# Performance work log

Measured on AMD Instinct MI355X. Metric: run time of the kernel, lower is better.

The kernel has to match this reference:

```python
import jax, jax.numpy as jnp
import numpy as np

N_NODES = 100000
N_EDGES = 3200000
N_GRAPHS = 512


def setup_inputs() -> dict:
    key = jax.random.key(0)
    k1, k2, k3, k4, k5 = jax.random.split(key, 5)
    x = jax.random.normal(k1, (N_NODES, 5), dtype=jnp.float32)
    edge_index = jax.random.randint(k2, (2, N_EDGES), 0, N_NODES, dtype=jnp.int64)
    batch = jnp.sort(jax.random.randint(k3, (N_NODES,), 0, N_GRAPHS, dtype=jnp.int64))
    W1 = jax.random.normal(k4, (5, 16), dtype=jnp.float32) * (1.0 / np.sqrt(5.0))
    b1 = jnp.zeros((16,), dtype=jnp.float32)
    W2 = jax.random.normal(k5, (16, 16), dtype=jnp.float32) * 0.25
    b2 = jnp.zeros((16,), dtype=jnp.float32)
    return {"x": x, "edge_index": edge_index, "batch": batch,
            "W1": W1, "b1": b1, "W2": W2, "b2": b2}


def _gcn_conv(x, src, dst, norm, W, b, n_nodes):
    # PyG GCNConv: h = X W; out_i = sum_{j->i} norm_ij * h_j + b
    h = x @ W                                   # [N, out]
    msgs = h[src] * norm[:, None]               # gather + scale  [E_tot, out]
    out = jax.ops.segment_sum(msgs, dst, num_segments=n_nodes)
    return out + b


def reference(x, edge_index, batch, W1, b1, W2, b2):
    n = x.shape[0]
    # add self-loops (GCNConv default)
    loops = jnp.arange(n, dtype=edge_index.dtype)
    src = jnp.concatenate([edge_index[0], loops])
    dst = jnp.concatenate([edge_index[1], loops])
    # symmetric normalization: deg computed on destination nodes
    deg = jax.ops.segment_sum(jnp.ones_like(src, dtype=x.dtype), dst, num_segments=n)
    dinv = jnp.where(deg > 0, jax.lax.rsqrt(deg), 0.0)
    norm = dinv[src] * dinv[dst]                # [E_tot]

    h = jax.nn.relu(_gcn_conv(x, src, dst, norm, W1, b1, n))
    h = jax.nn.relu(_gcn_conv(h, src, dst, norm, W2, b2, n))

    # global mean pool over graphs in the batch
    sums = jax.ops.segment_sum(h, batch, num_segments=N_GRAPHS)
    cnts = jax.ops.segment_sum(jnp.ones((n,), dtype=h.dtype), batch, num_segments=N_GRAPHS)
    return sums / jnp.maximum(cnts, 1.0)[:, None]
```

## Files before the change

### kernel.cpp

```cpp
#include <hip/hip_runtime.h>

#define N_NODES  100000
#define N_EDGES  3200000
#define N_GRAPHS 512
#define F_IN     5
#define F_HID    16

#define PBLK   512
#define CHUNK  4096
#define EPT    (CHUNK / PBLK)
#define NCHUNK ((N_EDGES + CHUNK - 1) / CHUNK)
#define CNT_NODES 128
#define BKT_NODES 256
#define NBKT ((N_NODES + BKT_NODES - 1) / BKT_NODES)
#define SHARDS 8
#define CAP_S  1280
#define CAP    (SHARDS * CAP_S)
#define UNR    (CAP / 512)


__device__ inline unsigned short f2bf(float f) {
    unsigned u = __float_as_uint(f);
    return (unsigned short)((u + 0x7fffu + ((u >> 16) & 1u)) >> 16);
}
__device__ inline float bf2f(unsigned short h) {
    return __uint_as_float(((unsigned)h) << 16);
}
__device__ inline float4 cvt4(ushort4 u) {
    return make_float4(bf2f(u.x), bf2f(u.y), bf2f(u.z), bf2f(u.w));
}
__device__ inline float4 shfl_xor4(float4 v, int m) {
    return make_float4(__shfl_xor(v.x, m, 64), __shfl_xor(v.y, m, 64),
                       __shfl_xor(v.z, m, 64), __shfl_xor(v.w, m, 64));
}

template <int NW>
__device__ inline int block_incl_scan(int v, int t, int* wsum) {
    int lane = t & 63, wave = t >> 6;
    int x = v;
#pragma unroll
    for (int o = 1; o < 64; o <<= 1) {
        int y = __shfl_up(x, o, 64);
        if (lane >= o) x += y;
    }
    if (lane == 63) wsum[wave] = x;
    __syncthreads();
    if (t < 64) {
        int w = (t < NW) ? wsum[t] : 0;
#pragma unroll
        for (int o = 1; o < NW; o <<= 1) {
            int y = __shfl_up(w, o, 64);
            if (t >= o) w += y;
        }
        if (t < NW) wsum[t] = w;
    }
    __syncthreads();
    return x + (wave ? wsum[wave - 1] : 0);
}

__device__ inline float4 row_gather8s(const ushort4* __restrict__ pb4, int i, int j,
                                      int half, int beg, int len,
                                      const int* __restrict__ col) {
    float4 acc = half ? make_float4(0.f, 0.f, 0.f, 0.f)
                      : cvt4(pb4[i * 4 + j]);
    for (int k = half * 8; k < len; k += 16) {
        int4 c0 = *(const int4*)(col + beg + k);
        int4 c1 = *(const int4*)(col + beg + k + 4);
        ushort4 a0 = pb4[c0.x * 4 + j], a1 = pb4[c0.y * 4 + j];
        ushort4 a2 = pb4[c0.z * 4 + j], a3 = pb4[c0.w * 4 + j];
        ushort4 a4 = pb4[c1.x * 4 + j], a5 = pb4[c1.y * 4 + j];
        ushort4 a6 = pb4[c1.z * 4 + j], a7 = pb4[c1.w * 4 + j];
        float4 f0 = cvt4(a0), f1 = cvt4(a1), f2 = cvt4(a2), f3 = cvt4(a3);
        float4 f4 = cvt4(a4), f5 = cvt4(a5), f6 = cvt4(a6), f7 = cvt4(a7);
        acc.x += ((f0.x + f1.x) + (f2.x + f3.x)) + ((f4.x + f5.x) + (f6.x + f7.x));
        acc.y += ((f0.y + f1.y) + (f2.y + f3.y)) + ((f4.y + f5.y) + (f6.y + f7.y));
        acc.z += ((f0.z + f1.z) + (f2.z + f3.z)) + ((f4.z + f5.z) + (f6.z + f7.z));
        acc.w += ((f0.w + f1.w) + (f2.w + f3.w)) + ((f4.w + f5.w) + (f6.w + f7.w));
    }
    return acc;
}


__global__ void k_zero(int* __restrict__ cursor, float* __restrict__ out,
                       float* __restrict__ cnt, unsigned short* __restrict__ pb_a,
                       unsigned short* __restrict__ pb_b) {
    int i = blockIdx.x * blockDim.x + threadIdx.x;
    if (i < NBKT * SHARDS) cursor[i] = 0;
    if (i < N_GRAPHS * F_HID) out[i] = 0.0f;
    if (i < N_GRAPHS) cnt[i] = 0.0f;
    if (i < F_HID) {
        pb_a[(size_t)N_NODES * F_HID + i] = 0;
        pb_b[(size_t)N_NODES * F_HID + i] = 0;
    }
}

__global__ __launch_bounds__(PBLK) void k_part(const int* __restrict__ src,
                                               const int* __restrict__ dst,
                                               const int* __restrict__ batch,
                                               int* __restrict__ cursor,
                                               unsigned* __restrict__ packed,
                                               float* __restrict__ cnt) {
    __shared__ int hist[PBLK];
    __shared__ int gbase[PBLK];
    __shared__ int bcnt[8];
    __shared__ int g0s;
    int t = threadIdx.x;
    int blk = blockIdx.x;
    int s = blk & (SHARDS - 1);
    int chunk0 = blk * CHUNK;
    int n = min(CHUNK, N_EDGES - chunk0);
    hist[t] = 0;
    if (t < 8) bcnt[t] = 0;
    if (t == 0) {
        int nb = blk * CNT_NODES;
        g0s = batch[nb < N_NODES ? nb : N_NODES - 1];
    }
    __syncthreads();
    int ls[EPT], ld[EPT], lr[EPT];
#pragma unroll
    for (int idx = 0; idx < EPT; idx++) {
        int k = t + idx * PBLK;
        if (k < n) {
            ls[idx] = src[chunk0 + k];
            ld[idx] = dst[chunk0 + k];
            lr[idx] = atomicAdd(&hist[ld[idx] >> 8], 1);
        }
    }
    if (t < CNT_NODES) {
        int i2 = blk * CNT_NODES + t;
        if (i2 < N_NODES) {
            int g = batch[i2];
            int l = g - g0s;
            if (l >= 0 && l < 8) atomicAdd(&bcnt[l], 1);
            else atomicAdd(&cnt[g], 1.0f);
        }
    }
    __syncthreads();
    int v = hist[t];
    gbase[t] = (v > 0) ? atomicAdd(&cursor[t * SHARDS + s], v) : 0;
    if (t < 8 && bcnt[t] > 0) atomicAdd(&cnt[g0s + t], (float)bcnt[t]);
    __syncthreads();
#pragma unroll
    for (int idx = 0; idx < EPT; idx++) {
        int k = t + idx * PBLK;
        if (k < n) {
            int b = ld[idx] >> 8;
            int g = gbase[b] + lr[idx];
            if (g < CAP_S)
                packed[(size_t)b * CAP + s * CAP_S + g] =
                    ((unsigned)ls[idx] << 8) | (unsigned)(ld[idx] & 255);
        }
    }
}

__global__ __launch_bounds__(512) void k_csr(const int* __restrict__ cursor,
                                             const unsigned* __restrict__ packed,
                                             const float* __restrict__ x,
                                             const float* __restrict__ W1,
                                             int2* __restrict__ rowbc,
                                             int* __restrict__ col,
                                             float* __restrict__ dinv,
                                             unsigned short* __restrict__ pb) {
    __shared__ int hist[BKT_NODES];
    __shared__ int excl_s[BKT_NODES];
    __shared__ int wsum[8];
    __shared__ int ns[SHARDS];
    __shared__ float w1[F_IN * F_HID];
    int b = blockIdx.x, t = threadIdx.x;
    int base = b * CAP;
    if (t < BKT_NODES) hist[t] = 0;
    if (t < SHARDS) ns[t] = min(cursor[b * SHARDS + t], CAP_S);
    if (t < F_IN * F_HID) w1[t] = W1[t];
    __syncthreads();
    const unsigned* pk = packed + (size_t)b * CAP;
    unsigned pv[UNR];
    int pr[UNR];
    unsigned okm = 0;
#pragma unroll
    for (int idx = 0; idx < UNR; idx++) {
        int k = t + idx * 512;
        int sh = k / CAP_S;
        if ((k - sh * CAP_S) < ns[sh]) {
            okm |= (1u << idx);
            pv[idx] = pk[k];
            pr[idx] = atomicAdd(&hist[pv[idx] & 255], 1);
        }
    }
    __syncthreads();
    int v = (t < BKT_NODES) ? hist[t] : 0;
    int len = (v + 7) & ~7;
    int incl = block_incl_scan<8>(len, t, wsum);
    int excl = incl - len;
    if (t < BKT_NODES) excl_s[t] = excl;
    __syncthreads();
#pragma unroll
    for (int idx = 0; idx < UNR; idx++) {
        if (okm & (1u << idx)) {
            unsigned w = pv[idx];
            int r = excl_s[w & 255] + pr[idx];
            if (r < CAP) col[base + r] = (int)(w >> 8);
        }
    }
    if (t < BKT_NODES) {
        int node = b * BKT_NODES + t;
        if (node < N_NODES) {
            int mylen = min(len, ((CAP - min(excl, CAP)) & ~7));
            for (int q = v; q < mylen; q++) {
                int r = excl + q;
                if (r < CAP) col[base + r] = N_NODES;
            }
            rowbc[node] = make_int2(base + excl, mylen);
            float di = rsqrtf((float)(1 + v));
            dinv[node] = di;
            float xi[F_IN];
#pragma unroll
            for (int k = 0; k < F_IN; k++) xi[k] = x[node * F_IN + k];
            float hv[F_HID];
#pragma unroll
            for (int c = 0; c < F_HID; c++) {
                float h = 0.0f;
#pragma unroll
                for (int k = 0; k < F_IN; k++) h += xi[k] * w1[k * F_HID + c];
                hv[c] = h * di;
            }
            unsigned pkk[8];
#pragma unroll
            for (int q = 0; q < 8; q++)
                pkk[q] = (unsigned)f2bf(hv[2 * q]) | ((unsigned)f2bf(hv[2 * q + 1]) << 16);
            uint4* d4 = (uint4*)(pb + (size_t)node * F_HID);
            d4[0] = make_uint4(pkk[0], pkk[1], pkk[2], pkk[3]);
            d4[1] = make_uint4(pkk[4], pkk[5], pkk[6], pkk[7]);
        }
    }
}

__global__ __launch_bounds__(256) void k_pull_mid(const int2* __restrict__ rowbc,
                                                  const int* __restrict__ col,
                                                  const unsigned short* __restrict__ pb,
                                                  const float* __restrict__ dinv,
                                                  const float* __restrict__ W2,
                                                  const float* __restrict__ b1,
                                                  unsigned short* __restrict__ pb2) {
    __shared__ float w[F_HID * F_HID];
    __shared__ float bb[F_HID];
    int t = threadIdx.x;
    w[t] = W2[t];
    if (t < F_HID) bb[t] = b1[t];
    __syncthreads();
    int gid = blockIdx.x * 256 + t;
    int i = gid >> 3;
    int half = (gid >> 2) & 1;
    int j = gid & 3;
    int2 rc = rowbc[i];
    float4 acc = row_gather8s((const ushort4*)pb, i, j, half, rc.x, rc.y, col);
    acc.x += __shfl_xor(acc.x, 4, 64);
    acc.y += __shfl_xor(acc.y, 4, 64);
    acc.z += __shfl_xor(acc.z, 4, 64);
    acc.w += __shfl_xor(acc.w, 4, 64);
    float di = dinv[i];
    float4 mine;
    mine.x = fmaxf(di * acc.x + bb[4 * j + 0], 0.0f);
    mine.y = fmaxf(di * acc.y + bb[4 * j + 1], 0.0f);
    mine.z = fmaxf(di * acc.z + bb[4 * j + 2], 0.0f);
    mine.w = fmaxf(di * acc.w + bb[4 * j + 3], 0.0f);
    float4 o1 = shfl_xor4(mine, 1);
    float4 o2 = shfl_xor4(mine, 2);
    float4 o3 = shfl_xor4(mine, 3);
    float4 hq0 = (j == 0) ? mine : ((j == 1) ? o1 : ((j == 2) ? o2 : o3));
    float4 hq1 = (j == 1) ? mine : ((j == 0) ? o1 : ((j == 3) ? o2 : o3));
    float4 hq2 = (j == 2) ? mine : ((j == 3) ? o1 : ((j == 0) ? o2 : o3));
    float4 hq3 = (j == 3) ? mine : ((j == 2) ? o1 : ((j == 1) ? o2 : o3));
    float hc[F_HID] = {hq0.x, hq0.y, hq0.z, hq0.w, hq1.x, hq1.y, hq1.z, hq1.w,
                       hq2.x, hq2.y, hq2.z, hq2.w, hq3.x, hq3.y, hq3.z, hq3.w};
    float m0 = 0.0f, m1 = 0.0f, m2 = 0.0f, m3 = 0.0f;
#pragma unroll
    for (int c = 0; c < F_HID; c++) {
        float4 wv = *(const float4*)&w[c * F_HID + 4 * j];
        float hv = hc[c];
        m0 += hv * wv.x; m1 += hv * wv.y; m2 += hv * wv.z; m3 += hv * wv.w;
    }
    if (half == 0) {
        unsigned p0 = (unsigned)f2bf(m0 * di) | ((unsigned)f2bf(m1 * di) << 16);
        unsigned p1 = (unsigned)f2bf(m2 * di) | ((unsigned)f2bf(m3 * di) << 16);
        *(uint2*)(pb2 + (size_t)i * F_HID + 4 * j) = make_uint2(p0, p1);
    }
}

__global__ __launch_bounds__(256) void k_pull_pool(const int2* __restrict__ rowbc,
                                                   const int* __restrict__ col,
                                                   const unsigned short* __restrict__ pb,
                                                   const float* __restrict__ dinv,
                                                   const int* __restrict__ batch,
                                                   const float* __restrict__ b2,
                                                   const float* __restrict__ cnt,
                                                   float* __restrict__ out) {
    __shared__ float bb[F_HID];
    __shared__ float acc2[8][F_HID];
    __shared__ int gcnt[8];
    __shared__ int g0s;
    int t = threadIdx.x;
    if (t < F_HID) bb[t] = b2[t];
    if (t < 8) gcnt[t] = 0;
    if (t < 8 * F_HID) ((float*)acc2)[t] = 0.0f;
    int blk0node = blockIdx.x * 32;
    if (t == 0) g0s = batch[blk0node < N_NODES ? blk0node : N_NODES - 1];
    __syncthreads();
    int g0 = g0s;
    int gid = blockIdx.x * 256 + t;
    int i = gid >> 3;
    int half = (gid >> 2) & 1;
    int j = gid & 3;
    int2 rc = rowbc[i];
    float4 acc = row_gather8s((const ushort4*)pb, i, j, half, rc.x, rc.y, col);
    acc.x += __shfl_xor(acc.x, 4, 64);
    acc.y += __shfl_xor(acc.y, 4, 64);
    acc.z += __shfl_xor(acc.z, 4, 64);
    acc.w += __shfl_xor(acc.w, 4, 64);
    if (half == 0) {
        float di = dinv[i];
        float h0 = fmaxf(di * acc.x + bb[4 * j + 0], 0.0f);
        float h1 = fmaxf(di * acc.y + bb[4 * j + 1], 0.0f);
        float h2 = fmaxf(di * acc.z + bb[4 * j + 2], 0.0f);
        float h3 = fmaxf(di * acc.w + bb[4 * j + 3], 0.0f);
        int g = batch[i];
        int l = g - g0;
        if (l >= 0 && l < 8) {
            atomicAdd(&acc2[l][4 * j + 0], h0);
            atomicAdd(&acc2[l][4 * j + 1], h1);
            atomicAdd(&acc2[l][4 * j + 2], h2);
            atomicAdd(&acc2[l][4 * j + 3], h3);
            if (j == 0) atomicAdd(&gcnt[l], 1);
        } else {
            float inv = 1.0f / cnt[g];
            atomicAdd(&out[g * F_HID + 4 * j + 0], h0 * inv);
            atomicAdd(&out[g * F_HID + 4 * j + 1], h1 * inv);
            atomicAdd(&out[g * F_HID + 4 * j + 2], h2 * inv);
            atomicAdd(&out[g * F_HID + 4 * j + 3], h3 * inv);
        }
    }
    __syncthreads();
    if (t < 8 * F_HID) {
        int l = t >> 4, c = t & 15;
        if (gcnt[l] > 0) {
            float inv = 1.0f / cnt[g0 + l];
            atomicAdd(&out[(g0 + l) * F_HID + c], acc2[l][c] * inv);
        }
    }
}


extern "C" void kernel_launch(void* const* d_in, const int* in_sizes, int n_in,
                              void* d_out, int out_size, void* d_ws, size_t ws_size,
                              hipStream_t stream) {
    const float* x     = (const float*)d_in[0];
    const int*   ei    = (const int*)d_in[1];
    const int*   batch = (const int*)d_in[2];
    const float* W1    = (const float*)d_in[3];
    const float* b1    = (const float*)d_in[4];
    const float* W2    = (const float*)d_in[5];
    const float* b2    = (const float*)d_in[6];
    float* out = (float*)d_out;

    int*            cursor = (int*)d_ws;
    unsigned*       packed = (unsigned*)(cursor + 3200);
    int2*           rowbc  = (int2*)(packed + (size_t)NBKT * CAP);
    int*            col    = (int*)(rowbc + N_NODES);
    float*          dinv   = (float*)(col + (size_t)NBKT * CAP);
    unsigned short* pb_a   = (unsigned short*)(dinv + N_NODES);
    unsigned short* pb_b   = pb_a + (size_t)(N_NODES + 1) * F_HID;
    float*          cnt    = (float*)(pb_b + (size_t)(N_NODES + 1) * F_HID);

    const int* src = ei;
    const int* dst = ei + N_EDGES;

    const int nb_pull = (N_NODES * 8) / 256;

    k_zero<<<(N_GRAPHS * F_HID + 255) / 256, 256, 0, stream>>>(cursor, out, cnt,
                                                               pb_a, pb_b);
    k_part<<<NCHUNK, PBLK, 0, stream>>>(src, dst, batch, cursor, packed, cnt);
    k_csr<<<NBKT, 512, 0, stream>>>(cursor, packed, x, W1, rowbc, col, dinv, pb_a);
    k_pull_mid<<<nb_pull, 256, 0, stream>>>(rowbc, col, pb_a, dinv, W2, b1, pb_b);
    k_pull_pool<<<nb_pull, 256, 0, stream>>>(rowbc, col, pb_b, dinv, batch, b2,
                                             cnt, out);
}
```

Before: 190.0 us.

## Fuse GCN pipeline into one cooperative persistent kernel with grid syncs

Merges the zero, partition, CSR-build and two pull kernels into a single cooperative kernel. The phases are separated by grid.sync, and persistent blocks loop over chunks, buckets and windows. The goal is to remove the launch and inter-kernel drain gaps between the five stages. Buckets and chunks are halved, blocks drop to 256 threads, and CSR construction now reads packed edges twice with atomic ranking instead of caching them in registers. Risks include grid-sync cost, lower occupancy from capping resident blocks at four per CU during the latency-bound gather phases, and the extra packed reads; a non-cooperative multi-kernel fallback is kept.

```diff
diff --git a/kernel.cpp b/kernel.cpp
--- a/kernel.cpp
+++ b/kernel.cpp
@@ -1,4 +1,7 @@
 #include <hip/hip_runtime.h>
+#include <hip/hip_cooperative_groups.h>
+
+namespace cg = cooperative_groups;
 
 #define N_NODES  100000
 #define N_EDGES  3200000
@@ -6,17 +9,18 @@
 #define F_IN     5
 #define F_HID    16
 
-#define PBLK   512
-#define CHUNK  4096
-#define EPT    (CHUNK / PBLK)
+#define NTHR   256
+#define CHUNK  2048
+#define EPT    (CHUNK / NTHR)
 #define NCHUNK ((N_EDGES + CHUNK - 1) / CHUNK)
-#define CNT_NODES 128
-#define BKT_NODES 256
+#define CNT_NODES 64
+#define BKT_NODES 128
+#define BKT_SHIFT 7
 #define NBKT ((N_NODES + BKT_NODES - 1) / BKT_NODES)
 #define SHARDS 8
-#define CAP_S  1280
+#define CAP_S  768
 #define CAP    (SHARDS * CAP_S)
-#define UNR    (CAP / 512)
+#define NWIN   (N_NODES / 32)
 
 
 __device__ inline unsigned short f2bf(float f) {
@@ -34,8 +38,7 @@
                        __shfl_xor(v.z, m, 64), __shfl_xor(v.w, m, 64));
 }
 
-template <int NW>
-__device__ inline int block_incl_scan(int v, int t, int* wsum) {
+__device__ inline int scan128(int v, int t, int* wsum) {
     int lane = t & 63, wave = t >> 6;
     int x = v;
 #pragma unroll
@@ -46,13 +49,13 @@
     if (lane == 63) wsum[wave] = x;
     __syncthreads();
     if (t < 64) {
-        int w = (t < NW) ? wsum[t] : 0;
-#pragma unroll
-        for (int o = 1; o < NW; o <<= 1) {
+        int w = (t < 4) ? wsum[t] : 0;
+#pragma unroll
+        for (int o = 1; o < 4; o <<= 1) {
             int y = __shfl_up(w, o, 64);
             if (t >= o) w += y;
         }
-        if (t < NW) wsum[t] = w;
+        if (t < 4) wsum[t] = w;
     }
     __syncthreads();
     return x + (wave ? wsum[wave - 1] : 0);
@@ -81,53 +84,39 @@
 }
 
 
-__global__ void k_zero(int* __restrict__ cursor, float* __restrict__ out,
-                       float* __restrict__ cnt, unsigned short* __restrict__ pb_a,
-                       unsigned short* __restrict__ pb_b) {
-    int i = blockIdx.x * blockDim.x + threadIdx.x;
-    if (i < NBKT * SHARDS) cursor[i] = 0;
-    if (i < N_GRAPHS * F_HID) out[i] = 0.0f;
-    if (i < N_GRAPHS) cnt[i] = 0.0f;
-    if (i < F_HID) {
-        pb_a[(size_t)N_NODES * F_HID + i] = 0;
-        pb_b[(size_t)N_NODES * F_HID + i] = 0;
-    }
-}
-
-__global__ __launch_bounds__(PBLK) void k_part(const int* __restrict__ src,
-                                               const int* __restrict__ dst,
-                                               const int* __restrict__ batch,
-                                               int* __restrict__ cursor,
-                                               unsigned* __restrict__ packed,
-                                               float* __restrict__ cnt) {
-    __shared__ int hist[PBLK];
-    __shared__ int gbase[PBLK];
+__device__ inline void phase_part(int c, const int* __restrict__ src,
+                                  const int* __restrict__ dst,
+                                  const int* __restrict__ batch,
+                                  int* __restrict__ cursor,
+                                  unsigned* __restrict__ packed,
+                                  float* __restrict__ cnt) {
+    __shared__ int hist[NBKT];
+    __shared__ int gbase[NBKT];
     __shared__ int bcnt[8];
     __shared__ int g0s;
     int t = threadIdx.x;
-    int blk = blockIdx.x;
-    int s = blk & (SHARDS - 1);
-    int chunk0 = blk * CHUNK;
+    int s = c & (SHARDS - 1);
+    int chunk0 = c * CHUNK;
     int n = min(CHUNK, N_EDGES - chunk0);
-    hist[t] = 0;
+    for (int i = t; i < NBKT; i += NTHR) hist[i] = 0;
     if (t < 8) bcnt[t] = 0;
     if (t == 0) {
-        int nb = blk * CNT_NODES;
+        int nb = c * CNT_NODES;
         g0s = batch[nb < N_NODES ? nb : N_NODES - 1];
     }
     __syncthreads();
     int ls[EPT], ld[EPT], lr[EPT];
 #pragma unroll
     for (int idx = 0; idx < EPT; idx++) {
-        int k = t + idx * PBLK;
+        int k = t + idx * NTHR;
         if (k < n) {
             ls[idx] = src[chunk0 + k];
             ld[idx] = dst[chunk0 + k];
-            lr[idx] = atomicAdd(&hist[ld[idx] >> 8], 1);
+            lr[idx] = atomicAdd(&hist[ld[idx] >> BKT_SHIFT], 1);
         }
     }
     if (t < CNT_NODES) {
-        int i2 = blk * CNT_NODES + t;
+        int i2 = c * CNT_NODES + t;
         if (i2 < N_NODES) {
             int g = batch[i2];
             int l = g - g0s;
@@ -136,69 +125,68 @@
         }
     }
     __syncthreads();
-    int v = hist[t];
-    gbase[t] = (v > 0) ? atomicAdd(&cursor[t * SHARDS + s], v) : 0;
+    for (int b = t; b < NBKT; b += NTHR) {
+        int v = hist[b];
+        gbase[b] = (v > 0) ? atomicAdd(&cursor[b * SHARDS + s], v) : 0;
+    }
     if (t < 8 && bcnt[t] > 0) atomicAdd(&cnt[g0s + t], (float)bcnt[t]);
     __syncthreads();
 #pragma unroll
     for (int idx = 0; idx < EPT; idx++) {
-        int k = t + idx * PBLK;
+        int k = t + idx * NTHR;
         if (k < n) {
-            int b = ld[idx] >> 8;
+            int b = ld[idx] >> BKT_SHIFT;
             int g = gbase[b] + lr[idx];
             if (g < CAP_S)
                 packed[(size_t)b * CAP + s * CAP_S + g] =
-                    ((unsigned)ls[idx] << 8) | (unsigned)(ld[idx] & 255);
-        }
-    }
-}
-
-__global__ __launch_bounds__(512) void k_csr(const int* __restrict__ cursor,
-                                             const unsigned* __restrict__ packed,
-                                             const float* __restrict__ x,
-                                             const float* __restrict__ W1,
-                                             int2* __restrict__ rowbc,
-                                             int* __restrict__ col,
-                                             float* __restrict__ dinv,
-                                             unsigned short* __restrict__ pb) {
-    __shared__ int hist[BKT_NODES];
-    __shared__ int excl_s[BKT_NODES];
-    __shared__ int wsum[8];
+                    ((unsigned)ls[idx] << BKT_SHIFT) |
+                    (unsigned)(ld[idx] & (BKT_NODES - 1));
+        }
+    }
+    __syncthreads();
+}
+
+__device__ inline void phase_csr(int b, const int* __restrict__ cursor,
+                                 const unsigned* __restrict__ packed,
+                                 const float* __restrict__ x,
+                                 const float* __restrict__ W1,
+                                 int2* __restrict__ rowbc, int* __restrict__ col,
+                                 float* __restrict__ dinv,
+                                 unsigned short* __restrict__ pb) {
+    __shared__ int chist[BKT_NODES];
+    __shared__ int crnk[BKT_NODES];
+    __shared__ int wsum[4];
     __shared__ int ns[SHARDS];
     __shared__ float w1[F_IN * F_HID];
-    int b = blockIdx.x, t = threadIdx.x;
+    int t = threadIdx.x;
     int base = b * CAP;
-    if (t < BKT_NODES) hist[t] = 0;
+    if (t < BKT_NODES) chist[t] = 0;
     if (t < SHARDS) ns[t] = min(cursor[b * SHARDS + t], CAP_S);
     if (t < F_IN * F_HID) w1[t] = W1[t];
     __syncthreads();
     const unsigned* pk = packed + (size_t)b * CAP;
-    unsigned pv[UNR];
-    int pr[UNR];
-    unsigned okm = 0;
-#pragma unroll
-    for (int idx = 0; idx < UNR; idx++) {
-        int k = t + idx * 512;
-        int sh = k / CAP_S;
-        if ((k - sh * CAP_S) < ns[sh]) {
-            okm |= (1u << idx);
-            pv[idx] = pk[k];
-            pr[idx] = atomicAdd(&hist[pv[idx] & 255], 1);
-        }
-    }
-    __syncthreads();
-    int v = (t < BKT_NODES) ? hist[t] : 0;
+#pragma unroll
+    for (int s = 0; s < SHARDS; s++) {
+        int m = ns[s];
+        const unsigned* pks = pk + s * CAP_S;
+        for (int k = t; k < m; k += NTHR)
+            atomicAdd(&chist[pks[k] & (BKT_NODES - 1)], 1);
+    }
+    __syncthreads();
+    int v = (t < BKT_NODES) ? chist[t] : 0;
     int len = (v + 7) & ~7;
-    int incl = block_incl_scan<8>(len, t, wsum);
+    int incl = scan128(len, t, wsum);
     int excl = incl - len;
-    if (t < BKT_NODES) excl_s[t] = excl;
-    __syncthreads();
-#pragma unroll
-    for (int idx = 0; idx < UNR; idx++) {
-        if (okm & (1u << idx)) {
-            unsigned w = pv[idx];
-            int r = excl_s[w & 255] + pr[idx];
-            if (r < CAP) col[base + r] = (int)(w >> 8);
+    if (t < BKT_NODES) crnk[t] = excl;
+    __syncthreads();
+#pragma unroll
+    for (int s = 0; s < SHARDS; s++) {
+        int m = ns[s];
+        const unsigned* pks = pk + s * CAP_S;
+        for (int k = t; k < m; k += NTHR) {
+            unsigned w = pks[k];
+            int r = atomicAdd(&crnk[w & (BKT_NODES - 1)], 1);
+            if (r < CAP) col[base + r] = (int)(w >> BKT_SHIFT);
         }
     }
     if (t < BKT_NODES) {
@@ -226,31 +214,31 @@
             unsigned pkk[8];
 #pragma unroll
             for (int q = 0; q < 8; q++)
-                pkk[q] = (unsigned)f2bf(hv[2 * q]) | ((unsigned)f2bf(hv[2 * q + 1]) << 16);
+                pkk[q] = (unsigned)f2bf(hv[2 * q]) |
+                         ((unsigned)f2bf(hv[2 * q + 1]) << 16);
             uint4* d4 = (uint4*)(pb + (size_t)node * F_HID);
             d4[0] = make_uint4(pkk[0], pkk[1], pkk[2], pkk[3]);
             d4[1] = make_uint4(pkk[4], pkk[5], pkk[6], pkk[7]);
         }
     }
-}
-
-__global__ __launch_bounds__(256) void k_pull_mid(const int2* __restrict__ rowbc,
-                                                  const int* __restrict__ col,
-                                                  const unsigned short* __restrict__ pb,
-                                                  const float* __restrict__ dinv,
-                                                  const float* __restrict__ W2,
-                                                  const float* __restrict__ b1,
-                                                  unsigned short* __restrict__ pb2) {
-    __shared__ float w[F_HID * F_HID];
-    __shared__ float bb[F_HID];
+    __syncthreads();
+}
+
+__device__ inline void phase_mid(int w, const int2* __restrict__ rowbc,
+                                 const int* __restrict__ col,
+                                 const unsigned short* __restrict__ pb,
+                                 const float* __restrict__ dinv,
+                                 const float* __restrict__ W2,
+                                 const float* __restrict__ b1,
+                                 unsigned short* __restrict__ pb2) {
+    __shared__ float w2s[F_HID * F_HID];
+    __shared__ float bb1[F_HID];
     int t = threadIdx.x;
-    w[t] = W2[t];
-    if (t < F_HID) bb[t] = b1[t];
-    __syncthreads();
-    int gid = blockIdx.x * 256 + t;
-    int i = gid >> 3;
-    int half = (gid >> 2) & 1;
-    int j = gid & 3;
+    w2s[t] = W2[t];
+    if (t < F_HID) bb1[t] = b1[t];
+    __syncthreads();
+    int half = (t >> 2) & 1, j = t & 3, nl = t >> 3;
+    int i = w * 32 + nl;
     int2 rc = rowbc[i];
     float4 acc = row_gather8s((const ushort4*)pb, i, j, half, rc.x, rc.y, col);
     acc.x += __shfl_xor(acc.x, 4, 64);
@@ -259,10 +247,10 @@
     acc.w += __shfl_xor(acc.w, 4, 64);
     float di = dinv[i];
     float4 mine;
-    mine.x = fmaxf(di * acc.x + bb[4 * j + 0], 0.0f);
-    mine.y = fmaxf(di * acc.y + bb[4 * j + 1], 0.0f);
-    mine.z = fmaxf(di * acc.z + bb[4 * j + 2], 0.0f);
-    mine.w = fmaxf(di * acc.w + bb[4 * j + 3], 0.0f);
+    mine.x = fmaxf(di * acc.x + bb1[4 * j + 0], 0.0f);
+    mine.y = fmaxf(di * acc.y + bb1[4 * j + 1], 0.0f);
+    mine.z = fmaxf(di * acc.z + bb1[4 * j + 2], 0.0f);
+    mine.w = fmaxf(di * acc.w + bb1[4 * j + 3], 0.0f);
     float4 o1 = shfl_xor4(mine, 1);
     float4 o2 = shfl_xor4(mine, 2);
     float4 o3 = shfl_xor4(mine, 3);
@@ -275,7 +263,7 @@
     float m0 = 0.0f, m1 = 0.0f, m2 = 0.0f, m3 = 0.0f;
 #pragma unroll
     for (int c = 0; c < F_HID; c++) {
-        float4 wv = *(const float4*)&w[c * F_HID + 4 * j];
+        float4 wv = *(const float4*)&w2s[c * F_HID + 4 * j];
         float hv = hc[c];
         m0 += hv * wv.x; m1 += hv * wv.y; m2 += hv * wv.z; m3 += hv * wv.w;
     }
@@ -284,32 +272,30 @@
         unsigned p1 = (unsigned)f2bf(m2 * di) | ((unsigned)f2bf(m3 * di) << 16);
         *(uint2*)(pb2 + (size_t)i * F_HID + 4 * j) = make_uint2(p0, p1);
     }
-}
-
-__global__ __launch_bounds__(256) void k_pull_pool(const int2* __restrict__ rowbc,
-                                                   const int* __restrict__ col,
-                                                   const unsigned short* __restrict__ pb,
-                                                   const float* __restrict__ dinv,
-                                                   const int* __restrict__ batch,
-                                                   const float* __restrict__ b2,
-                                                   const float* __restrict__ cnt,
-                                                   float* __restrict__ out) {
-    __shared__ float bb[F_HID];
+    __syncthreads();
+}
+
+__device__ inline void phase_pool(int w, const int2* __restrict__ rowbc,
+                                  const int* __restrict__ col,
+                                  const unsigned short* __restrict__ pb,
+                                  const float* __restrict__ dinv,
+                                  const int* __restrict__ batch,
+                                  const float* __restrict__ b2,
+                                  const float* __restrict__ cnt,
+                                  float* __restrict__ out) {
+    __shared__ float bb2[F_HID];
     __shared__ float acc2[8][F_HID];
     __shared__ int gcnt[8];
-    __shared__ int g0s;
+    __shared__ int pg0;
     int t = threadIdx.x;
-    if (t < F_HID) bb[t] = b2[t];
+    if (t < F_HID) bb2[t] = b2[t];
     if (t < 8) gcnt[t] = 0;
     if (t < 8 * F_HID) ((float*)acc2)[t] = 0.0f;
-    int blk0node = blockIdx.x * 32;
-    if (t == 0) g0s = batch[blk0node < N_NODES ? blk0node : N_NODES - 1];
-    __syncthreads();
-    int g0 = g0s;
-    int gid = blockIdx.x * 256 + t;
-    int i = gid >> 3;
-    int half = (gid >> 2) & 1;
-    int j = gid & 3;
+    if (t == 0) pg0 = batch[w * 32];
+    __syncthreads();
+    int g0 = pg0;
+    int half = (t >> 2) & 1, j = t & 3, nl = t >> 3;
+    int i = w * 32 + nl;
     int2 rc = rowbc[i];
     float4 acc = row_gather8s((const ushort4*)pb, i, j, half, rc.x, rc.y, col);
     acc.x += __shfl_xor(acc.x, 4, 64);
@@ -318,10 +304,10 @@
     acc.w += __shfl_xor(acc.w, 4, 64);
     if (half == 0) {
         float di = dinv[i];
-        float h0 = fmaxf(di * acc.x + bb[4 * j + 0], 0.0f);
-        float h1 = fmaxf(di * acc.y + bb[4 * j + 1], 0.0f);
-        float h2 = fmaxf(di * acc.z + bb[4 * j + 2], 0.0f);
-        float h3 = fmaxf(di * acc.w + bb[4 * j + 3], 0.0f);
+        float h0 = fmaxf(di * acc.x + bb2[4 * j + 0], 0.0f);
+        float h1 = fmaxf(di * acc.y + bb2[4 * j + 1], 0.0f);
+        float h2 = fmaxf(di * acc.z + bb2[4 * j + 2], 0.0f);
+        float h3 = fmaxf(di * acc.w + bb2[4 * j + 3], 0.0f);
         int g = batch[i];
         int l = g - g0;
         if (l >= 0 && l < 8) {
@@ -346,6 +332,77 @@
             atomicAdd(&out[(g0 + l) * F_HID + c], acc2[l][c] * inv);
         }
     }
+    __syncthreads();
+}
+
+
+__global__ __launch_bounds__(NTHR, 4)
+void k_fused(const int* src, const int* dst, const int* batch, const float* x,
+             const float* W1, const float* b1, const float* W2, const float* b2,
+             int* cursor, unsigned* packed, int2* rowbc, int* col, float* dinv,
+             unsigned short* pb_a, unsigned short* pb_b, float* cnt, float* out) {
+    cg::grid_group grid = cg::this_grid();
+    int bid = blockIdx.x, t = threadIdx.x, nblk = gridDim.x;
+    int gstep = nblk * NTHR, gidx = bid * NTHR + t;
+    for (int i = gidx; i < NBKT * SHARDS; i += gstep) cursor[i] = 0;
+    for (int i = gidx; i < N_GRAPHS * F_HID; i += gstep) out[i] = 0.0f;
+    for (int i = gidx; i < N_GRAPHS; i += gstep) cnt[i] = 0.0f;
+    for (int i = gidx; i < F_HID; i += gstep) {
+        pb_a[(size_t)N_NODES * F_HID + i] = 0;
+        pb_b[(size_t)N_NODES * F_HID + i] = 0;
+    }
+    grid.sync();
+    for (int c = bid; c < NCHUNK; c += nblk)
+        phase_part(c, src, dst, batch, cursor, packed, cnt);
+    grid.sync();
+    for (int b = bid; b < NBKT; b += nblk)
+        phase_csr(b, cursor, packed, x, W1, rowbc, col, dinv, pb_a);
+    grid.sync();
+    for (int w = bid; w < NWIN; w += nblk)
+        phase_mid(w, rowbc, col, pb_a, dinv, W2, b1, pb_b);
+    grid.sync();
+    for (int w = bid; w < NWIN; w += nblk)
+        phase_pool(w, rowbc, col, pb_b, dinv, batch, b2, cnt, out);
+}
+
+
+__global__ __launch_bounds__(NTHR) void k_zero_s(int* cursor, float* out, float* cnt,
+                                                 unsigned short* pb_a,
+                                                 unsigned short* pb_b) {
+    int i = blockIdx.x * NTHR + threadIdx.x;
+    if (i < NBKT * SHARDS) cursor[i] = 0;
+    if (i < N_GRAPHS * F_HID) out[i] = 0.0f;
+    if (i < N_GRAPHS) cnt[i] = 0.0f;
+    if (i < F_HID) {
+        pb_a[(size_t)N_NODES * F_HID + i] = 0;
+        pb_b[(size_t)N_NODES * F_HID + i] = 0;
+    }
+}
+__global__ __launch_bounds__(NTHR) void k_part_s(const int* src, const int* dst,
+                                                 const int* batch, int* cursor,
+                                                 unsigned* packed, float* cnt) {
+    phase_part(blockIdx.x, src, dst, batch, cursor, packed, cnt);
+}
+__global__ __launch_bounds__(NTHR) void k_csr_s(const int* cursor,
+                                                const unsigned* packed,
+                                                const float* x, const float* W1,
+                                                int2* rowbc, int* col, float* dinv,
+                                                unsigned short* pb) {
+    phase_csr(blockIdx.x, cursor, packed, x, W1, rowbc, col, dinv, pb);
+}
+__global__ __launch_bounds__(NTHR) void k_mid_s(const int2* rowbc, const int* col,
+                                                const unsigned short* pb,
+                                                const float* dinv, const float* W2,
+                                                const float* b1,
+                                                unsigned short* pb2) {
+    phase_mid(blockIdx.x, rowbc, col, pb, dinv, W2, b1, pb2);
+}
+__global__ __launch_bounds__(NTHR) void k_pool_s(const int2* rowbc, const int* col,
+                                                 const unsigned short* pb,
+                                                 const float* dinv, const int* batch,
+                                                 const float* b2, const float* cnt,
+                                                 float* out) {
+    phase_pool(blockIdx.x, rowbc, col, pb, dinv, batch, b2, cnt, out);
 }
 
 
@@ -362,7 +419,7 @@
     float* out = (float*)d_out;
 
     int*            cursor = (int*)d_ws;
-    unsigned*       packed = (unsigned*)(cursor + 3200);
+    unsigned*       packed = (unsigned*)(cursor + 6400);
     int2*           rowbc  = (int2*)(packed + (size_t)NBKT * CAP);
     int*            col    = (int*)(rowbc + N_NODES);
     float*          dinv   = (float*)(col + (size_t)NBKT * CAP);
@@ -373,13 +430,29 @@
     const int* src = ei;
     const int* dst = ei + N_EDGES;
 
-    const int nb_pull = (N_NODES * 8) / 256;
-
-    k_zero<<<(N_GRAPHS * F_HID + 255) / 256, 256, 0, stream>>>(cursor, out, cnt,
-                                                               pb_a, pb_b);
-    k_part<<<NCHUNK, PBLK, 0, stream>>>(src, dst, batch, cursor, packed, cnt);
-    k_csr<<<NBKT, 512, 0, stream>>>(cursor, packed, x, W1, rowbc, col, dinv, pb_a);
-    k_pull_mid<<<nb_pull, 256, 0, stream>>>(rowbc, col, pb_a, dinv, W2, b1, pb_b);
-    k_pull_pool<<<nb_pull, 256, 0, stream>>>(rowbc, col, pb_b, dinv, batch, b2,
-                                             cnt, out);
-}
+    bool ok = false;
+    int maxBlk = 0;
+    hipError_t qe = hipOccupancyMaxActiveBlocksPerMultiprocessor(&maxBlk, k_fused,
+                                                                 NTHR, 0);
+    if (qe == hipSuccess && maxBlk > 0) {
+        int nblk = maxBlk * 256;
+        if (nblk > 1024) nblk = 1024;
+        void* args[] = {(void*)&src, (void*)&dst, (void*)&batch, (void*)&x,
+                        (void*)&W1, (void*)&b1, (void*)&W2, (void*)&b2,
+                        (void*)&cursor, (void*)&packed, (void*)&rowbc, (void*)&col,
+                        (void*)&dinv, (void*)&pb_a, (void*)&pb_b, (void*)&cnt,
+                        (void*)&out};
+        ok = hipLaunchCooperativeKernel((void*)k_fused, dim3(nblk), dim3(NTHR),
+                                        args, 0, stream) == hipSuccess;
+    }
+    if (!ok) {
+        k_zero_s<<<(N_GRAPHS * F_HID + NTHR - 1) / NTHR, NTHR, 0, stream>>>(
+            cursor, out, cnt, pb_a, pb_b);
+        k_part_s<<<NCHUNK, NTHR, 0, stream>>>(src, dst, batch, cursor, packed, cnt);
+        k_csr_s<<<NBKT, NTHR, 0, stream>>>(cursor, packed, x, W1, rowbc, col,
+                                           dinv, pb_a);
+        k_mid_s<<<NWIN, NTHR, 0, stream>>>(rowbc, col, pb_a, dinv, W2, b1, pb_b);
+        k_pool_s<<<NWIN, NTHR, 0, stream>>>(rowbc, col, pb_b, dinv, batch, b2,
+                                            cnt, out);
+    }
+}
```

Measured after the change: 524.4 us. 2.76x slower.

## Replicate bf16 feature tables per XCD and make CSR build two-pass

Applied to the files above, without the earlier changes.

Each bf16 node-feature table is now written as eight identical copies. Each gather block reads the copy chosen by blockIdx & 7, which lines up with the round-robin block-to-XCD assignment, so each XCD's L2 sees only its own copy. The goal is less cross-XCD contention on shared lines during the random row gathers, paid for with eight times the feature write traffic and workspace. Separately, k_csr stops holding packed edges in registers and rereads them in a second pass that places each edge with shared-memory atomics, and k_part's histogram is shrunk to the real bucket count.

```diff
diff --git a/kernel.cpp b/kernel.cpp
--- a/kernel.cpp
+++ b/kernel.cpp
@@ -17,6 +17,8 @@
 #define CAP_S  1280
 #define CAP    (SHARDS * CAP_S)
 #define UNR    (CAP / 512)
+#define NCOPY  8
+#define PBSTRIDE ((size_t)(N_NODES + 1) * F_HID)
 
 
 __device__ inline unsigned short f2bf(float f) {
@@ -88,9 +90,10 @@
     if (i < NBKT * SHARDS) cursor[i] = 0;
     if (i < N_GRAPHS * F_HID) out[i] = 0.0f;
     if (i < N_GRAPHS) cnt[i] = 0.0f;
-    if (i < F_HID) {
-        pb_a[(size_t)N_NODES * F_HID + i] = 0;
-        pb_b[(size_t)N_NODES * F_HID + i] = 0;
+    if (i < F_HID * NCOPY) {
+        int c = i / F_HID, q = i % F_HID;
+        pb_a[c * PBSTRIDE + (size_t)N_NODES * F_HID + q] = 0;
+        pb_b[c * PBSTRIDE + (size_t)N_NODES * F_HID + q] = 0;
     }
 }
 
@@ -100,8 +103,8 @@
                                                int* __restrict__ cursor,
                                                unsigned* __restrict__ packed,
                                                float* __restrict__ cnt) {
-    __shared__ int hist[PBLK];
-    __shared__ int gbase[PBLK];
+    __shared__ int hist[NBKT];
+    __shared__ int gbase[NBKT];
     __shared__ int bcnt[8];
     __shared__ int g0s;
     int t = threadIdx.x;
@@ -109,7 +112,7 @@
     int s = blk & (SHARDS - 1);
     int chunk0 = blk * CHUNK;
     int n = min(CHUNK, N_EDGES - chunk0);
-    hist[t] = 0;
+    if (t < NBKT) hist[t] = 0;
     if (t < 8) bcnt[t] = 0;
     if (t == 0) {
         int nb = blk * CNT_NODES;
@@ -136,8 +139,10 @@
         }
     }
     __syncthreads();
-    int v = hist[t];
-    gbase[t] = (v > 0) ? atomicAdd(&cursor[t * SHARDS + s], v) : 0;
+    if (t < NBKT) {
+        int v = hist[t];
+        gbase[t] = (v > 0) ? atomicAdd(&cursor[t * SHARDS + s], v) : 0;
+    }
     if (t < 8 && bcnt[t] > 0) atomicAdd(&cnt[g0s + t], (float)bcnt[t]);
     __syncthreads();
 #pragma unroll
@@ -162,7 +167,7 @@
                                              float* __restrict__ dinv,
                                              unsigned short* __restrict__ pb) {
     __shared__ int hist[BKT_NODES];
-    __shared__ int excl_s[BKT_NODES];
+    __shared__ int rnk[BKT_NODES];
     __shared__ int wsum[8];
     __shared__ int ns[SHARDS];
     __shared__ float w1[F_IN * F_HID];
@@ -173,31 +178,27 @@
     if (t < F_IN * F_HID) w1[t] = W1[t];
     __syncthreads();
     const unsigned* pk = packed + (size_t)b * CAP;
-    unsigned pv[UNR];
-    int pr[UNR];
-    unsigned okm = 0;
-#pragma unroll
-    for (int idx = 0; idx < UNR; idx++) {
-        int k = t + idx * 512;
-        int sh = k / CAP_S;
-        if ((k - sh * CAP_S) < ns[sh]) {
-            okm |= (1u << idx);
-            pv[idx] = pk[k];
-            pr[idx] = atomicAdd(&hist[pv[idx] & 255], 1);
-        }
+#pragma unroll
+    for (int s = 0; s < SHARDS; s++) {
+        int m = ns[s];
+        const unsigned* pks = pk + s * CAP_S;
+        for (int k = t; k < m; k += 512)
+            atomicAdd(&hist[pks[k] & 255], 1);
     }
     __syncthreads();
     int v = (t < BKT_NODES) ? hist[t] : 0;
     int len = (v + 7) & ~7;
     int incl = block_incl_scan<8>(len, t, wsum);
     int excl = incl - len;
-    if (t < BKT_NODES) excl_s[t] = excl;
-    __syncthreads();
-#pragma unroll
-    for (int idx = 0; idx < UNR; idx++) {
-        if (okm & (1u << idx)) {
-            unsigned w = pv[idx];
-            int r = excl_s[w & 255] + pr[idx];
+    if (t < BKT_NODES) rnk[t] = excl;
+    __syncthreads();
+#pragma unroll
+    for (int s = 0; s < SHARDS; s++) {
+        int m = ns[s];
+        const unsigned* pks = pk + s * CAP_S;
+        for (int k = t; k < m; k += 512) {
+            unsigned w = pks[k];
+            int r = atomicAdd(&rnk[w & 255], 1);
             if (r < CAP) col[base + r] = (int)(w >> 8);
         }
     }
@@ -227,9 +228,14 @@
 #pragma unroll
             for (int q = 0; q < 8; q++)
                 pkk[q] = (unsigned)f2bf(hv[2 * q]) | ((unsigned)f2bf(hv[2 * q + 1]) << 16);
-            uint4* d4 = (uint4*)(pb + (size_t)node * F_HID);
-            d4[0] = make_uint4(pkk[0], pkk[1], pkk[2], pkk[3]);
-            d4[1] = make_uint4(pkk[4], pkk[5], pkk[6], pkk[7]);
+            uint4 lo = make_uint4(pkk[0], pkk[1], pkk[2], pkk[3]);
+            uint4 hi4 = make_uint4(pkk[4], pkk[5], pkk[6], pkk[7]);
+#pragma unroll
+            for (int cp = 0; cp < NCOPY; cp++) {
+                uint4* d4 = (uint4*)(pb + cp * PBSTRIDE + (size_t)node * F_HID);
+                d4[0] = lo;
+                d4[1] = hi4;
+            }
         }
     }
 }
@@ -247,12 +253,13 @@
     w[t] = W2[t];
     if (t < F_HID) bb[t] = b1[t];
     __syncthreads();
+    const unsigned short* pbl = pb + (blockIdx.x & (NCOPY - 1)) * PBSTRIDE;
     int gid = blockIdx.x * 256 + t;
     int i = gid >> 3;
     int half = (gid >> 2) & 1;
     int j = gid & 3;
     int2 rc = rowbc[i];
-    float4 acc = row_gather8s((const ushort4*)pb, i, j, half, rc.x, rc.y, col);
+    float4 acc = row_gather8s((const ushort4*)pbl, i, j, half, rc.x, rc.y, col);
     acc.x += __shfl_xor(acc.x, 4, 64);
     acc.y += __shfl_xor(acc.y, 4, 64);
     acc.z += __shfl_xor(acc.z, 4, 64);
@@ -282,7 +289,10 @@
     if (half == 0) {
         unsigned p0 = (unsigned)f2bf(m0 * di) | ((unsigned)f2bf(m1 * di) << 16);
         unsigned p1 = (unsigned)f2bf(m2 * di) | ((unsigned)f2bf(m3 * di) << 16);
-        *(uint2*)(pb2 + (size_t)i * F_HID + 4 * j) = make_uint2(p0, p1);
+        uint2 pv = make_uint2(p0, p1);
+#pragma unroll
+        for (int cp = 0; cp < NCOPY; cp++)
+            *(uint2*)(pb2 + cp * PBSTRIDE + (size_t)i * F_HID + 4 * j) = pv;
     }
 }
 
@@ -305,13 +315,14 @@
     int blk0node = blockIdx.x * 32;
     if (t == 0) g0s = batch[blk0node < N_NODES ? blk0node : N_NODES - 1];
     __syncthreads();
+    const unsigned short* pbl = pb + (blockIdx.x & (NCOPY - 1)) * PBSTRIDE;
     int g0 = g0s;
     int gid = blockIdx.x * 256 + t;
     int i = gid >> 3;
     int half = (gid >> 2) & 1;
     int j = gid & 3;
     int2 rc = rowbc[i];
-    float4 acc = row_gather8s((const ushort4*)pb, i, j, half, rc.x, rc.y, col);
+    float4 acc = row_gather8s((const ushort4*)pbl, i, j, half, rc.x, rc.y, col);
     acc.x += __shfl_xor(acc.x, 4, 64);
     acc.y += __shfl_xor(acc.y, 4, 64);
     acc.z += __shfl_xor(acc.z, 4, 64);
@@ -367,8 +378,8 @@
     int*            col    = (int*)(rowbc + N_NODES);
     float*          dinv   = (float*)(col + (size_t)NBKT * CAP);
     unsigned short* pb_a   = (unsigned short*)(dinv + N_NODES);
-    unsigned short* pb_b   = pb_a + (size_t)(N_NODES + 1) * F_HID;
-    float*          cnt    = (float*)(pb_b + (size_t)(N_NODES + 1) * F_HID);
+    unsigned short* pb_b   = pb_a + NCOPY * PBSTRIDE;
+    float*          cnt    = (float*)(pb_b + NCOPY * PBSTRIDE);
 
     const int* src = ei;
     const int* dst = ei + N_EDGES;
```

Result: slower. 200.3 us (+5.4%).
